# Optimization experiments

Hardware: AMD Instinct MI355X
Metric: run time of the kernel (lower is better)

Reference implementation:

```python
import jax, jax.numpy as jnp
import numpy as np

NV, NC = 4096, 16384        # n_vars, n_clauses
VL, CL = 8, 8               # vlabel_dim (ground_dim), clabel_dim
VE, CE = 128, 128           # vemb_dim, cemb_dim
ITERS = 4                   # max_iters
LN_EPS = 1e-5


def setup_inputs() -> dict:
    key = jax.random.key(0)
    ks = jax.random.split(key, 10)
    return {
        "vlabels": jax.random.normal(ks[0], (NV, VL), jnp.float32),
        "clabels": jax.random.normal(ks[1], (NC, CL), jnp.float32),
        "cmat_pos": jax.random.uniform(ks[2], (NC, NV), jnp.float32),
        "cmat_neg": jax.random.uniform(ks[3], (NC, NV), jnp.float32),
        "W_V_pos": jax.random.normal(ks[4], (VL + VE, CE), jnp.float32),
        "W_V_neg": jax.random.normal(ks[5], (VL + VE, CE), jnp.float32),
        "B_V": jax.random.normal(ks[6], (CE,), jnp.float32),
        "W_C_pos": jax.random.normal(ks[7], (CL + CE, VE), jnp.float32),
        "W_C_neg": jax.random.normal(ks[8], (CL + CE, VE), jnp.float32),
        "B_C": jax.random.normal(ks[9], (VE,), jnp.float32),
        "ln_gamma": jnp.ones((VE,), jnp.float32),
        "ln_beta": jnp.zeros((VE,), jnp.float32),
    }


def _layernorm(x, gamma, beta):
    mu = jnp.mean(x, axis=-1, keepdims=True)
    var = jnp.var(x, axis=-1, keepdims=True)
    return (x - mu) * jax.lax.rsqrt(var + LN_EPS) * gamma + beta


def reference(vlabels, clabels, cmat_pos, cmat_neg,
              W_V_pos, W_V_neg, B_V, W_C_pos, W_C_neg, B_C,
              ln_gamma, ln_beta):
    n_vars = vlabels.shape[0]
    vmat_pos = cmat_pos.T  # [NV, NC]
    vmat_neg = cmat_neg.T
    vembs0 = jnp.zeros((n_vars, VE), vlabels.dtype)

    def step(vembs, _):
        vs = jnp.concatenate([vlabels, vembs], axis=1)          # [NV, VL+VE]
        pv = vs @ W_V_pos                                       # [NV, CE]
        nv = vs @ W_V_neg
        cembs = jax.nn.relu(cmat_pos @ pv + cmat_neg @ nv + B_V)  # [NC, CE]
        cs = jnp.concatenate([clabels, cembs], axis=1)          # [NC, CL+CE]
        pc = cs @ W_C_pos                                       # [NC, VE]
        nc = cs @ W_C_neg
        v = jax.nn.relu(vmat_pos @ pc + vmat_neg @ nc + B_C)    # [NV, VE]
        v = _layernorm(v, ln_gamma, ln_beta)
        return v, None

    vembs, _ = jax.lax.scan(step, vembs0, None, length=ITERS)
    return vembs
```

## Files before the change

### kernel.cpp

```cpp
#include <hip/hip_runtime.h>

#define NVV 4096
#define NCC 16384
#define AS1 __attribute__((address_space(1)))
#define AS3 __attribute__((address_space(3)))

typedef __attribute__((ext_vector_type(8))) short short8;
typedef __attribute__((ext_vector_type(4))) short short4v;
typedef __attribute__((ext_vector_type(4))) float f32x4;

__device__ __forceinline__ short f2bf(float f) {
  union { float f; unsigned u; } v; v.f = f;
  unsigned r = v.u + 0x7fffu + ((v.u >> 16) & 1u);
  return (short)(r >> 16);
}

template<typename AT>
__device__ __forceinline__ short8 load8v(const AT* p) {
  if constexpr (sizeof(AT) == 2) {
    return *(const short8*)p;
  } else {
    const f32x4* q = (const f32x4*)p;
    f32x4 a = q[0], b = q[1];
    short8 o;
#pragma unroll
    for (int j = 0; j < 4; ++j) { o[j] = f2bf(a[j]); o[j + 4] = f2bf(b[j]); }
    return o;
  }
}

__global__ __launch_bounds__(256) void k_conv(const float* __restrict__ src,
                                              short* __restrict__ dst, int n8) {
  int i = blockIdx.x * blockDim.x + threadIdx.x;
  const int stride = gridDim.x * blockDim.x;
  for (; i < n8; i += stride) {
    const f32x4* q = (const f32x4*)(src + (size_t)i * 8);
    f32x4 a = q[0], b = q[1];
    short8 o;
#pragma unroll
    for (int j = 0; j < 4; ++j) { o[j] = f2bf(a[j]); o[j + 4] = f2bf(b[j]); }
    *(short8*)(dst + (size_t)i * 8) = o;
  }
}

__global__ __launch_bounds__(256) void k_convT(const float* __restrict__ src,
                                               short* __restrict__ dstN,
                                               short* __restrict__ dstT,
                                               int R, int C) {
  __shared__ short t[64][66];
  const int r0 = blockIdx.y * 64, c0 = blockIdx.x * 64;
  const int tr = threadIdx.x >> 2;
  const int q  = (threadIdx.x & 3) << 4;
  const float* s = src + (size_t)(r0 + tr) * C + c0 + q;
  const f32x4 v0 = *(const f32x4*)(s);
  const f32x4 v1 = *(const f32x4*)(s + 4);
  const f32x4 v2 = *(const f32x4*)(s + 8);
  const f32x4 v3 = *(const f32x4*)(s + 12);
  short8 a, b;
#pragma unroll
  for (int j = 0; j < 4; ++j) {
    a[j] = f2bf(v0[j]); a[4 + j] = f2bf(v1[j]);
    b[j] = f2bf(v2[j]); b[4 + j] = f2bf(v3[j]);
  }
  short* dn = dstN + (size_t)(r0 + tr) * C + c0 + q;
  *(short8*)dn = a;
  *(short8*)(dn + 8) = b;
#pragma unroll
  for (int j = 0; j < 8; ++j) { t[tr][q + j] = a[j]; t[tr][q + 8 + j] = b[j]; }
  __syncthreads();
  short8 oa, ob;
#pragma unroll
  for (int j = 0; j < 8; ++j) { oa[j] = t[q + j][tr]; ob[j] = t[q + 8 + j][tr]; }
  short* dt = dstT + (size_t)(c0 + tr) * R + r0 + q;
  *(short8*)dt = oa;
  *(short8*)(dt + 8) = ob;
}

template<int SRC, int NROW>
__global__ __launch_bounds__(128) void k_mlp(
    const float* __restrict__ labels, const float* __restrict__ embs,
    const float* __restrict__ bias,
    const float* __restrict__ Wp, const float* __restrict__ Wn,
    short* __restrict__ Tp, short* __restrict__ Tn, int Nrows, int KS) {
  __shared__ float xs[NROW][130];
  const int n = threadIdx.x;
  const int m0 = blockIdx.x * NROW;
  if (SRC == 2) {
#pragma unroll
    for (int r = 0; r < NROW; ++r) {
      const size_t m = m0 + r;
      float v = bias[n];
      for (int ks = 0; ks < KS; ++ks)
        v += embs[((size_t)ks * NCC + m) * 128 + n];
      xs[r][n] = fmaxf(v, 0.f);
    }
    __syncthreads();
  }
  float ap[NROW] = {}, an[NROW] = {};
  const int JMAX = (SRC == 0) ? 8 : 136;
  for (int j = 0; j < JMAX; ++j) {
    const float wp = Wp[j * 128 + n], wn = Wn[j * 128 + n];
#pragma unroll
    for (int r = 0; r < NROW; ++r) {
      float x;
      if (j < 8)            x = labels[(size_t)(m0 + r) * 8 + j];
      else if (SRC == 2)    x = xs[r][j - 8];
      else                  x = embs[(size_t)(m0 + r) * 128 + (j - 8)];
      ap[r] = fmaf(x, wp, ap[r]);
      an[r] = fmaf(x, wn, an[r]);
    }
  }
  short8 vp0, vn0, vp1, vn1;
#pragma unroll
  for (int r = 0; r < 8; ++r) {
    vp0[r] = f2bf(ap[r]); vn0[r] = f2bf(an[r]);
    vp1[r] = f2bf(ap[8 + r]); vn1[r] = f2bf(an[8 + r]);
  }
  *(short8*)(Tp + (size_t)n * Nrows + m0) = vp0;
  *(short8*)(Tp + (size_t)n * Nrows + m0 + 8) = vp1;
  *(short8*)(Tn + (size_t)n * Nrows + m0) = vn0;
  *(short8*)(Tn + (size_t)n * Nrows + m0 + 8) = vn1;
}

template<int EPI, int LSK>
__global__ __launch_bounds__(256, 1) void k_gemm6(
    const short* __restrict__ Ap, const short* __restrict__ An,
    const short* __restrict__ Bp, const short* __restrict__ Bn,
    const float* __restrict__ bias, float* __restrict__ C,
    int M, int lda, int ldb, int Klen) {
  __shared__ __align__(16) short sb[4][12288];
  const int tid = threadIdx.x;
  const int w = tid >> 6, l = tid & 63, lr = l & 15, lh = l >> 4;
  const int wr = w >> 1, wc = w & 1;
  const int id = blockIdx.x;
  const int zw = id & ((1 << LSK) - 1);
  const int xw = id >> LSK;
  const int m0 = xw * 64;
  const int Koff = zw * Klen;
  const int T = (Klen >> 6) << 1;

  const int srow = tid >> 3;
  const int scol = ((tid & 7) ^ (srow & 7)) << 3;
  const short* gAp = Ap + (size_t)(m0 + srow) * lda + Koff + scol;
  const short* gAn = An + (size_t)(m0 + srow) * lda + Koff + scol;
  const short* gBp = Bp + (size_t)srow * ldb + Koff + scol;
  const short* gBn = Bn + (size_t)srow * ldb + Koff + scol;

  f32x4 acc[2][4] = {};

  auto stage = [&](int t, int buf) {
    const int tt = (t < T) ? t : t - T;
    const int k0 = (tt >> 1) << 6;
    const short* A = (tt & 1) ? gAn : gAp;
    const short* B = (tt & 1) ? gBn : gBp;
#pragma unroll
    for (int i = 0; i < 2; ++i)
      __builtin_amdgcn_global_load_lds(
          (const AS1 void*)(A + (size_t)(i * 32) * lda + k0),
          (AS3 void*)(&sb[buf][i * 2048 + w * 512]), 16, 0, 0);
#pragma unroll
    for (int i = 0; i < 4; ++i)
      __builtin_amdgcn_global_load_lds(
          (const AS1 void*)(B + (size_t)(i * 32) * ldb + k0),
          (AS3 void*)(&sb[buf][4096 + i * 2048 + w * 512]), 16, 0, 0);
  };

  stage(0, 0);
  stage(1, 1);

  for (int t = 0; t < T; ++t) {
    stage(t + 2, (t + 2) & 3);
    asm volatile("s_waitcnt vmcnt(12)" ::: "memory");
    __builtin_amdgcn_s_barrier();
    asm volatile("" ::: "memory");
    const short* bp = &sb[t & 3][0];
#pragma unroll
    for (int kk = 0; kk < 2; ++kk) {
      const int kc = (kk << 2) + lh;
      short8 a[2], b[4];
#pragma unroll
      for (int mi = 0; mi < 2; ++mi) {
        const int row = (wr << 5) + (mi << 4) + lr;
        a[mi] = *(const short8*)&bp[(row << 6) + ((kc ^ (row & 7)) << 3)];
      }
#pragma unroll
      for (int nj = 0; nj < 4; ++nj) {
        const int n = (wc << 6) + (nj << 4) + lr;
        b[nj] = *(const short8*)&bp[4096 + (n << 6) + ((kc ^ (n & 7)) << 3)];
      }
#pragma unroll
      for (int mi = 0; mi < 2; ++mi)
#pragma unroll
        for (int nj = 0; nj < 4; ++nj)
          acc[mi][nj] = __builtin_amdgcn_mfma_f32_16x16x32_bf16(
              a[mi], b[nj], acc[mi][nj], 0, 0, 0);
    }
  }

#pragma unroll
  for (int mi = 0; mi < 2; ++mi)
#pragma unroll
    for (int nj = 0; nj < 4; ++nj) {
      const int col = (wc << 6) + (nj << 4) + lr;
#pragma unroll
      for (int r = 0; r < 4; ++r) {
        const int m = m0 + (wr << 5) + (mi << 4) + (lh << 2) + r;
        if (EPI == 0) {
          C[(size_t)m * 128 + col] = fmaxf(acc[mi][nj][r] + bias[col], 0.f);
        } else {
          C[((size_t)zw * M + m) * 128 + col] = acc[mi][nj][r];
        }
      }
    }
}

template<typename AT, bool TRANSA, int EPI>
__global__ __launch_bounds__(256) void k_gemm(
    const AT* __restrict__ Ap, const AT* __restrict__ An,
    const short* __restrict__ Bp, const short* __restrict__ Bn,
    const float* __restrict__ bias, float* __restrict__ C,
    int M, int lda, int ldb, int Klen) {
  __shared__ __align__(16) short sA[2][32 * 64];
  __shared__ __align__(16) short sB[2][64 * 64];
  const int tid = threadIdx.x;
  const int w = tid >> 6, l = tid & 63, lr = l & 15, lh = l >> 4;
  const int m0 = blockIdx.x * 32, n0 = blockIdx.y * 64;
  const int Koff = blockIdx.z * Klen;
  f32x4 acc0 = {0.f, 0.f, 0.f, 0.f}, acc1 = {0.f, 0.f, 0.f, 0.f};

  for (int step = 0; step < (Klen >> 6); ++step) {
    const int k0 = Koff + (step << 6);
    __syncthreads();
    if (!TRANSA) {
      const int m = tid >> 3, kc = tid & 7;
      const size_t ga = (size_t)(m0 + m) * lda + k0 + (kc << 3);
      const int ad = (m << 6) + ((kc ^ (m & 7)) << 3);
      *(short8*)&sA[0][ad] = load8v(Ap + ga);
      *(short8*)&sA[1][ad] = load8v(An + ga);
    } else {
      const int r = tid >> 2, c8 = (tid & 3) << 3;
      const size_t ga = (size_t)(k0 + r) * lda + m0 + c8;
      short8 vp = load8v(Ap + ga), vn = load8v(An + ga);
#pragma unroll
      for (int j = 0; j < 8; ++j) {
        const int m = c8 + j;
        const int ad = (m << 6) + ((((r >> 3)) ^ (m & 7)) << 3) + (r & 7);
        sA[0][ad] = vp[j];
        sA[1][ad] = vn[j];
      }
    }
#pragma unroll
    for (int i = 0; i < 2; ++i) {
      const int c = (i << 8) + tid;
      const int n = c >> 3, kc = c & 7;
      const size_t gb = (size_t)(n0 + n) * ldb + k0 + (kc << 3);
      const int ad = (n << 6) + ((kc ^ (n & 7)) << 3);
      *(short8*)&sB[0][ad] = *(const short8*)(Bp + gb);
      *(short8*)&sB[1][ad] = *(const short8*)(Bn + gb);
    }
    __syncthreads();
#pragma unroll
    for (int kh = 0; kh < 2; ++kh) {
      const int kc = (kh << 2) + lh;
      const int bn_ = (w << 4) + lr;
      short8 bpv = *(short8*)&sB[0][(bn_ << 6) + ((kc ^ (bn_ & 7)) << 3)];
      short8 bnv = *(short8*)&sB[1][(bn_ << 6) + ((kc ^ (bn_ & 7)) << 3)];
      short8 a0p = *(short8*)&sA[0][(lr << 6) + ((kc ^ (lr & 7)) << 3)];
      short8 a0n = *(short8*)&sA[1][(lr << 6) + ((kc ^ (lr & 7)) << 3)];
      const int m1 = 16 + lr;
      short8 a1p = *(short8*)&sA[0][(m1 << 6) + ((kc ^ (m1 & 7)) << 3)];
      short8 a1n = *(short8*)&sA[1][(m1 << 6) + ((kc ^ (m1 & 7)) << 3)];
      acc0 = __builtin_amdgcn_mfma_f32_16x16x32_bf16(a0p, bpv, acc0, 0, 0, 0);
      acc0 = __builtin_amdgcn_mfma_f32_16x16x32_bf16(a0n, bnv, acc0, 0, 0, 0);
      acc1 = __builtin_amdgcn_mfma_f32_16x16x32_bf16(a1p, bpv, acc1, 0, 0, 0);
      acc1 = __builtin_amdgcn_mfma_f32_16x16x32_bf16(a1n, bnv, acc1, 0, 0, 0);
    }
  }
  const int n = n0 + (w << 4) + lr;
#pragma unroll
  for (int mf = 0; mf < 2; ++mf) {
    f32x4 a = mf ? acc1 : acc0;
#pragma unroll
    for (int r = 0; r < 4; ++r) {
      const int m = m0 + (mf << 4) + (lh << 2) + r;
      float c = a[r];
      if (EPI == 0) {
        c += bias[n];
        c = fmaxf(c, 0.f);
        C[(size_t)m * 128 + n] = c;
      } else {
        C[((size_t)blockIdx.z * M + m) * 128 + n] = c;
      }
    }
  }
}

template<int KS>
__global__ __launch_bounds__(256) void k_reduce_ln(
    const float* __restrict__ part, const float* __restrict__ bias,
    const float* __restrict__ gamma, const float* __restrict__ beta,
    float* __restrict__ out) {
  const int w = threadIdx.x >> 6, l = threadIdx.x & 63;
  const int m = blockIdx.x * 4 + w;
  const int n0 = l << 1;
  float x0 = bias[n0], x1 = bias[n0 + 1];
#pragma unroll
  for (int ks = 0; ks < KS; ++ks) {
    const size_t o = ((size_t)ks * NVV + m) * 128 + n0;
    x0 += part[o];
    x1 += part[o + 1];
  }
  x0 = fmaxf(x0, 0.f);
  x1 = fmaxf(x1, 0.f);
  float s = x0 + x1, q = x0 * x0 + x1 * x1;
#pragma unroll
  for (int off = 32; off; off >>= 1) {
    s += __shfl_xor(s, off);
    q += __shfl_xor(q, off);
  }
  const float mu = s * (1.f / 128.f);
  const float var = q * (1.f / 128.f) - mu * mu;
  const float inv = 1.f / sqrtf(var + 1e-5f);
  out[(size_t)m * 128 + n0]     = (x0 - mu) * inv * gamma[n0] + beta[n0];
  out[(size_t)m * 128 + n0 + 1] = (x1 - mu) * inv * gamma[n0 + 1] + beta[n0 + 1];
}

extern "C" void kernel_launch(void* const* d_in, const int* in_sizes, int n_in,
                              void* d_out, int out_size, void* d_ws, size_t ws_size,
                              hipStream_t stream) {
  const float* vlabels  = (const float*)d_in[0];
  const float* clabels  = (const float*)d_in[1];
  const float* cmat_pos = (const float*)d_in[2];
  const float* cmat_neg = (const float*)d_in[3];
  const float* Wvp = (const float*)d_in[4];
  const float* Wvn = (const float*)d_in[5];
  const float* Bv  = (const float*)d_in[6];
  const float* Wcp = (const float*)d_in[7];
  const float* Wcn = (const float*)d_in[8];
  const float* Bc  = (const float*)d_in[9];
  const float* gam = (const float*)d_in[10];
  const float* bet = (const float*)d_in[11];
  float* out = (float*)d_out;

  char* base = (char*)d_ws;
  const size_t SZ_vT = (size_t)128 * NVV * 2;
  const size_t SZ_cT = (size_t)128 * NCC * 2;
  const size_t SZ_cm = (size_t)NCC * NVV * 2;
  const size_t SZ_p8 = (size_t)NCC * 128 * 4;

  size_t o = 0;
  auto al = [&](size_t b) { size_t p = o; o += (b + 255) & ~(size_t)255; return p; };

  short* pvT  = (short*)(base + al(SZ_vT));
  short* nvT  = (short*)(base + al(SZ_vT));
  short* pcT  = (short*)(base + al(SZ_cT));
  short* ncT  = (short*)(base + al(SZ_cT));
  float* scr8 = (float*)(base + al(SZ_p8));
  short* cmPb = (short*)(base + al(SZ_cm));
  short* cmNb = (short*)(base + al(SZ_cm));
  short* cmTP = (short*)(base + al(SZ_cm));
  short* cmTN = (short*)(base + al(SZ_cm));
  const size_t needF = o;

  if (ws_size >= needF) {
    k_convT<<<dim3(NVV / 64, NCC / 64), 256, 0, stream>>>(cmat_pos, cmPb, cmTP, NCC, NVV);
    k_convT<<<dim3(NVV / 64, NCC / 64), 256, 0, stream>>>(cmat_neg, cmNb, cmTN, NCC, NVV);

    for (int it = 0; it < 4; ++it) {
      if (it == 0)
        k_mlp<0, 16><<<NVV / 16, 128, 0, stream>>>(vlabels, nullptr, nullptr, Wvp, Wvn, pvT, nvT, NVV, 0);
      else
        k_mlp<1, 16><<<NVV / 16, 128, 0, stream>>>(vlabels, out, nullptr, Wvp, Wvn, pvT, nvT, NVV, 0);

      k_gemm6<0, 0><<<NCC / 64, 256, 0, stream>>>(
          cmPb, cmNb, pvT, nvT, Bv, scr8, NCC, NVV, NVV, NVV);

      k_mlp<1, 16><<<NCC / 16, 128, 0, stream>>>(clabels, scr8, nullptr, Wcp, Wcn, pcT, ncT, NCC, 0);

      k_gemm6<1, 2><<<(NVV / 64) * 4, 256, 0, stream>>>(
          cmTP, cmTN, pcT, ncT, nullptr, scr8, NVV, NCC, NCC, NCC / 4);

      k_reduce_ln<4><<<NVV / 4, 256, 0, stream>>>(scr8, Bc, gam, bet, out);
    }
    return;
  }

  o = 0;
  pvT = (short*)(base + al(SZ_vT));
  nvT = (short*)(base + al(SZ_vT));
  pcT = (short*)(base + al(SZ_cT));
  ncT = (short*)(base + al(SZ_cT));
  float* part = (float*)(base + al(2 * SZ_p8));
  float* cemb = (float*)(base + al(SZ_p8));
  cmPb = (short*)(base + al(SZ_cm));
  cmNb = (short*)(base + al(SZ_cm));
  const size_t needN = o;
  const bool big = ws_size >= needN;

  if (big) {
    k_conv<<<4096, 256, 0, stream>>>(cmat_pos, cmPb, NCC * NVV / 8);
    k_conv<<<4096, 256, 0, stream>>>(cmat_neg, cmNb, NCC * NVV / 8);
  }

  for (int it = 0; it < 4; ++it) {
    if (it == 0)
      k_mlp<0, 16><<<NVV / 16, 128, 0, stream>>>(vlabels, nullptr, nullptr, Wvp, Wvn, pvT, nvT, NVV, 0);
    else
      k_mlp<1, 16><<<NVV / 16, 128, 0, stream>>>(vlabels, out, nullptr, Wvp, Wvn, pvT, nvT, NVV, 0);

    if (big) {
      k_gemm<short, false, 0><<<dim3(NCC / 32, 2, 1), 256, 0, stream>>>(
          cmPb, cmNb, pvT, nvT, Bv, cemb, NCC, NVV, NVV, NVV);
      k_mlp<1, 16><<<NCC / 16, 128, 0, stream>>>(clabels, cemb, nullptr, Wcp, Wcn, pcT, ncT, NCC, 0);
      k_gemm<short, true, 1><<<dim3(NVV / 32, 2, 4), 256, 0, stream>>>(
          cmPb, cmNb, pcT, ncT, nullptr, part, NVV, NVV, NCC, NVV);
      k_reduce_ln<4><<<NVV / 4, 256, 0, stream>>>(part, Bc, gam, bet, out);
    } else {
      k_gemm<float, false, 0><<<dim3(NCC / 32, 2, 1), 256, 0, stream>>>(
          cmat_pos, cmat_neg, pvT, nvT, Bv, cemb, NCC, NVV, NVV, NVV);
      k_mlp<1, 16><<<NCC / 16, 128, 0, stream>>>(clabels, cemb, nullptr, Wcp, Wcn, pcT, ncT, NCC, 0);
      k_gemm<float, true, 1><<<dim3(NVV / 32, 2, 4), 256, 0, stream>>>(
          cmat_pos, cmat_neg, pcT, ncT, nullptr, part, NVV, NVV, NCC, NVV);
      k_reduce_ln<4><<<NVV / 4, 256, 0, stream>>>(part, Bc, gam, bet, out);
    }
  }
}
```

Baseline: 1.382 ms.

## Replace GEMM with 128-row tiles, split-K for both passes, fused pos/neg stages

The bf16 MFMA GEMM now uses 128x128 output tiles with K-step 32, double-buffered LDS, and loads both pos and neg A/B tiles into each stage. Occupancy is raised to 2 blocks per CU. Both sparse-style products now use split-K (4 and 16 ways), which puts 512 blocks on the GPU. The clause bias+ReLU moves into the MLP kernel, which reduces the partials. The MLP kernel also stages embeddings through LDS. The costs are larger partial-sum scratch buffers and extra reduction traffic, and each step waits on vmcnt(0), so loads overlap with compute less.

```diff
diff --git a/kernel.cpp b/kernel.cpp
--- a/kernel.cpp
+++ b/kernel.cpp
@@ -82,10 +82,15 @@
     const float* __restrict__ bias,
     const float* __restrict__ Wp, const float* __restrict__ Wn,
     short* __restrict__ Tp, short* __restrict__ Tn, int Nrows, int KS) {
-  __shared__ float xs[NROW][130];
+  __shared__ float xs[NROW][129];
   const int n = threadIdx.x;
   const int m0 = blockIdx.x * NROW;
-  if (SRC == 2) {
+  if (SRC == 1) {
+#pragma unroll
+    for (int r = 0; r < NROW; ++r)
+      xs[r][n] = embs[(size_t)(m0 + r) * 128 + n];
+    __syncthreads();
+  } else if (SRC == 2) {
 #pragma unroll
     for (int r = 0; r < NROW; ++r) {
       const size_t m = m0 + r;
@@ -103,9 +108,8 @@
 #pragma unroll
     for (int r = 0; r < NROW; ++r) {
       float x;
-      if (j < 8)            x = labels[(size_t)(m0 + r) * 8 + j];
-      else if (SRC == 2)    x = xs[r][j - 8];
-      else                  x = embs[(size_t)(m0 + r) * 128 + (j - 8)];
+      if (j < 8) x = labels[(size_t)(m0 + r) * 8 + j];
+      else       x = xs[r][j - 8];
       ap[r] = fmaf(x, wp, ap[r]);
       an[r] = fmaf(x, wn, an[r]);
     }
@@ -122,94 +126,94 @@
   *(short8*)(Tn + (size_t)n * Nrows + m0 + 8) = vn1;
 }
 
-template<int EPI, int LSK>
-__global__ __launch_bounds__(256, 1) void k_gemm6(
+template<int LSK>
+__global__ __launch_bounds__(256, 2) void k_gemm8(
     const short* __restrict__ Ap, const short* __restrict__ An,
     const short* __restrict__ Bp, const short* __restrict__ Bn,
-    const float* __restrict__ bias, float* __restrict__ C,
-    int M, int lda, int ldb, int Klen) {
-  __shared__ __align__(16) short sb[4][12288];
+    float* __restrict__ C, int M, int lda, int ldb, int Klen) {
+  __shared__ __align__(16) short sb[2][16384];
   const int tid = threadIdx.x;
   const int w = tid >> 6, l = tid & 63, lr = l & 15, lh = l >> 4;
   const int wr = w >> 1, wc = w & 1;
   const int id = blockIdx.x;
   const int zw = id & ((1 << LSK) - 1);
-  const int xw = id >> LSK;
-  const int m0 = xw * 64;
+  const int m0 = (id >> LSK) * 128;
   const int Koff = zw * Klen;
-  const int T = (Klen >> 6) << 1;
-
-  const int srow = tid >> 3;
-  const int scol = ((tid & 7) ^ (srow & 7)) << 3;
+  const int T = Klen >> 5;
+
+  const int srow = (w << 4) + (l >> 2);
+  const int scol = ((l & 3) ^ (srow & 3)) << 3;
   const short* gAp = Ap + (size_t)(m0 + srow) * lda + Koff + scol;
   const short* gAn = An + (size_t)(m0 + srow) * lda + Koff + scol;
   const short* gBp = Bp + (size_t)srow * ldb + Koff + scol;
   const short* gBn = Bn + (size_t)srow * ldb + Koff + scol;
 
-  f32x4 acc[2][4] = {};
-
-  auto stage = [&](int t, int buf) {
-    const int tt = (t < T) ? t : t - T;
-    const int k0 = (tt >> 1) << 6;
-    const short* A = (tt & 1) ? gAn : gAp;
-    const short* B = (tt & 1) ? gBn : gBp;
-#pragma unroll
-    for (int i = 0; i < 2; ++i)
-      __builtin_amdgcn_global_load_lds(
-          (const AS1 void*)(A + (size_t)(i * 32) * lda + k0),
-          (AS3 void*)(&sb[buf][i * 2048 + w * 512]), 16, 0, 0);
-#pragma unroll
-    for (int i = 0; i < 4; ++i)
-      __builtin_amdgcn_global_load_lds(
-          (const AS1 void*)(B + (size_t)(i * 32) * ldb + k0),
-          (AS3 void*)(&sb[buf][4096 + i * 2048 + w * 512]), 16, 0, 0);
+  f32x4 acc[4][4] = {};
+
+  auto stage = [&](int kstep, int buf) {
+    const int k0 = kstep << 5;
+    short* db = &sb[buf][0];
+#pragma unroll
+    for (int i = 0; i < 2; ++i) {
+      const size_t ra = (size_t)(i * 64) * lda + k0;
+      const size_t rb = (size_t)(i * 64) * ldb + k0;
+      const int d = (i * 256 + w * 64) * 8;
+      __builtin_amdgcn_global_load_lds((const AS1 void*)(gAp + ra),
+                                       (AS3 void*)(db + d), 16, 0, 0);
+      __builtin_amdgcn_global_load_lds((const AS1 void*)(gAn + ra),
+                                       (AS3 void*)(db + 4096 + d), 16, 0, 0);
+      __builtin_amdgcn_global_load_lds((const AS1 void*)(gBp + rb),
+                                       (AS3 void*)(db + 8192 + d), 16, 0, 0);
+      __builtin_amdgcn_global_load_lds((const AS1 void*)(gBn + rb),
+                                       (AS3 void*)(db + 12288 + d), 16, 0, 0);
+    }
   };
 
   stage(0, 0);
-  stage(1, 1);
+  asm volatile("s_waitcnt vmcnt(0)" ::: "memory");
+  __builtin_amdgcn_s_barrier();
+  asm volatile("" ::: "memory");
 
   for (int t = 0; t < T; ++t) {
-    stage(t + 2, (t + 2) & 3);
-    asm volatile("s_waitcnt vmcnt(12)" ::: "memory");
+    stage((t + 1 < T) ? t + 1 : 0, (t + 1) & 1);
+    const short* bp = &sb[t & 1][0];
+    short8 a[2][4], b[2][4];
+#pragma unroll
+    for (int mi = 0; mi < 4; ++mi) {
+      const int row = (wr << 6) + (mi << 4) + lr;
+      const int ad = (row << 5) + ((lh ^ (row & 3)) << 3);
+      a[0][mi] = *(const short8*)&bp[ad];
+      a[1][mi] = *(const short8*)&bp[4096 + ad];
+    }
+#pragma unroll
+    for (int nj = 0; nj < 4; ++nj) {
+      const int n = (wc << 6) + (nj << 4) + lr;
+      const int bd = (n << 5) + ((lh ^ (n & 3)) << 3);
+      b[0][nj] = *(const short8*)&bp[8192 + bd];
+      b[1][nj] = *(const short8*)&bp[12288 + bd];
+    }
+#pragma unroll
+    for (int mat = 0; mat < 2; ++mat)
+#pragma unroll
+      for (int mi = 0; mi < 4; ++mi)
+#pragma unroll
+        for (int nj = 0; nj < 4; ++nj)
+          acc[mi][nj] = __builtin_amdgcn_mfma_f32_16x16x32_bf16(
+              a[mat][mi], b[mat][nj], acc[mi][nj], 0, 0, 0);
+    asm volatile("s_waitcnt vmcnt(0)" ::: "memory");
     __builtin_amdgcn_s_barrier();
     asm volatile("" ::: "memory");
-    const short* bp = &sb[t & 3][0];
-#pragma unroll
-    for (int kk = 0; kk < 2; ++kk) {
-      const int kc = (kk << 2) + lh;
-      short8 a[2], b[4];
-#pragma unroll
-      for (int mi = 0; mi < 2; ++mi) {
-        const int row = (wr << 5) + (mi << 4) + lr;
-        a[mi] = *(const short8*)&bp[(row << 6) + ((kc ^ (row & 7)) << 3)];
-      }
-#pragma unroll
-      for (int nj = 0; nj < 4; ++nj) {
-        const int n = (wc << 6) + (nj << 4) + lr;
-        b[nj] = *(const short8*)&bp[4096 + (n << 6) + ((kc ^ (n & 7)) << 3)];
-      }
-#pragma unroll
-      for (int mi = 0; mi < 2; ++mi)
-#pragma unroll
-        for (int nj = 0; nj < 4; ++nj)
-          acc[mi][nj] = __builtin_amdgcn_mfma_f32_16x16x32_bf16(
-              a[mi], b[nj], acc[mi][nj], 0, 0, 0);
-    }
-  }
-
-#pragma unroll
-  for (int mi = 0; mi < 2; ++mi)
+  }
+
+#pragma unroll
+  for (int mi = 0; mi < 4; ++mi)
 #pragma unroll
     for (int nj = 0; nj < 4; ++nj) {
       const int col = (wc << 6) + (nj << 4) + lr;
 #pragma unroll
       for (int r = 0; r < 4; ++r) {
-        const int m = m0 + (wr << 5) + (mi << 4) + (lh << 2) + r;
-        if (EPI == 0) {
-          C[(size_t)m * 128 + col] = fmaxf(acc[mi][nj][r] + bias[col], 0.f);
-        } else {
-          C[((size_t)zw * M + m) * 128 + col] = acc[mi][nj][r];
-        }
+        const int m = m0 + (wr << 6) + (mi << 4) + (lh << 2) + r;
+        C[((size_t)zw * M + m) * 128 + col] = acc[mi][nj][r];
       }
     }
 }
@@ -355,7 +359,7 @@
   short* nvT  = (short*)(base + al(SZ_vT));
   short* pcT  = (short*)(base + al(SZ_cT));
   short* ncT  = (short*)(base + al(SZ_cT));
-  float* scr8 = (float*)(base + al(SZ_p8));
+  float* scr  = (float*)(base + al(4 * SZ_p8));
   short* cmPb = (short*)(base + al(SZ_cm));
   short* cmNb = (short*)(base + al(SZ_cm));
   short* cmTP = (short*)(base + al(SZ_cm));
@@ -372,15 +376,13 @@
       else
         k_mlp<1, 16><<<NVV / 16, 128, 0, stream>>>(vlabels, out, nullptr, Wvp, Wvn, pvT, nvT, NVV, 0);
 
-      k_gemm6<0, 0><<<NCC / 64, 256, 0, stream>>>(
-          cmPb, cmNb, pvT, nvT, Bv, scr8, NCC, NVV, NVV, NVV);
-
-      k_mlp<1, 16><<<NCC / 16, 128, 0, stream>>>(clabels, scr8, nullptr, Wcp, Wcn, pcT, ncT, NCC, 0);
-
-      k_gemm6<1, 2><<<(NVV / 64) * 4, 256, 0, stream>>>(
-          cmTP, cmTN, pcT, ncT, nullptr, scr8, NVV, NCC, NCC, NCC / 4);
-
-      k_reduce_ln<4><<<NVV / 4, 256, 0, stream>>>(scr8, Bc, gam, bet, out);
+      k_gemm8<2><<<512, 256, 0, stream>>>(
+          cmPb, cmNb, pvT, nvT, scr, NCC, NVV, NVV, NVV / 4);
+      k_mlp<2, 16><<<NCC / 16, 128, 0, stream>>>(clabels, scr, Bv, Wcp, Wcn, pcT, ncT, NCC, 4);
+
+      k_gemm8<4><<<512, 256, 0, stream>>>(
+          cmTP, cmTN, pcT, ncT, scr, NVV, NCC, NCC, NCC / 16);
+      k_reduce_ln<16><<<NVV / 4, 256, 0, stream>>>(scr, Bc, gam, bet, out);
     }
     return;
   }
```

Measured after the change: 1.558 ms. +12.8%, slower.

## Split-K both GEMMs to 512 blocks with 3-stage pipeline and 2 blocks/CU

Applied to the files above, without the earlier changes.

The clause GEMM becomes split-K by 2, with bias and relu applied in the following MLP, which sums the partials. The variable GEMM becomes split-K by 8 instead of 4. Each launch now uses 512 blocks, so work spreads across more CUs. The LDS ring drops from 4 to 3 buffers with prefetch depth 1 so that two blocks fit per CU, and the MLP stages vembs into shared memory. The cost is extra partial-sum traffic and reduction work, plus a shallower prefetch that may expose load latency.

```diff
diff --git a/kernel.cpp b/kernel.cpp
--- a/kernel.cpp
+++ b/kernel.cpp
@@ -82,10 +82,15 @@
     const float* __restrict__ bias,
     const float* __restrict__ Wp, const float* __restrict__ Wn,
     short* __restrict__ Tp, short* __restrict__ Tn, int Nrows, int KS) {
-  __shared__ float xs[NROW][130];
+  __shared__ float xs[NROW][129];
   const int n = threadIdx.x;
   const int m0 = blockIdx.x * NROW;
-  if (SRC == 2) {
+  if (SRC == 1) {
+#pragma unroll
+    for (int r = 0; r < NROW; ++r)
+      xs[r][n] = embs[(size_t)(m0 + r) * 128 + n];
+    __syncthreads();
+  } else if (SRC == 2) {
 #pragma unroll
     for (int r = 0; r < NROW; ++r) {
       const size_t m = m0 + r;
@@ -103,9 +108,8 @@
 #pragma unroll
     for (int r = 0; r < NROW; ++r) {
       float x;
-      if (j < 8)            x = labels[(size_t)(m0 + r) * 8 + j];
-      else if (SRC == 2)    x = xs[r][j - 8];
-      else                  x = embs[(size_t)(m0 + r) * 128 + (j - 8)];
+      if (j < 8) x = labels[(size_t)(m0 + r) * 8 + j];
+      else       x = xs[r][j - 8];
       ap[r] = fmaf(x, wp, ap[r]);
       an[r] = fmaf(x, wn, an[r]);
     }
@@ -123,19 +127,18 @@
 }
 
 template<int EPI, int LSK>
-__global__ __launch_bounds__(256, 1) void k_gemm6(
+__global__ __launch_bounds__(256, 2) void k_gemm10(
     const short* __restrict__ Ap, const short* __restrict__ An,
     const short* __restrict__ Bp, const short* __restrict__ Bn,
     const float* __restrict__ bias, float* __restrict__ C,
     int M, int lda, int ldb, int Klen) {
-  __shared__ __align__(16) short sb[4][12288];
+  __shared__ __align__(16) short sb[3][12288];
   const int tid = threadIdx.x;
   const int w = tid >> 6, l = tid & 63, lr = l & 15, lh = l >> 4;
   const int wr = w >> 1, wc = w & 1;
   const int id = blockIdx.x;
   const int zw = id & ((1 << LSK) - 1);
-  const int xw = id >> LSK;
-  const int m0 = xw * 64;
+  const int m0 = (id >> LSK) * 64;
   const int Koff = zw * Klen;
   const int T = (Klen >> 6) << 1;
 
@@ -166,14 +169,16 @@
   };
 
   stage(0, 0);
-  stage(1, 1);
-
+
+  int bufc = 0;
+  const int r0 = lr, r1 = 16 + lr;
   for (int t = 0; t < T; ++t) {
-    stage(t + 2, (t + 2) & 3);
-    asm volatile("s_waitcnt vmcnt(12)" ::: "memory");
+    const int bufn = (bufc == 2) ? 0 : bufc + 1;
+    stage(t + 1, bufn);
+    asm volatile("s_waitcnt vmcnt(6)" ::: "memory");
     __builtin_amdgcn_s_barrier();
     asm volatile("" ::: "memory");
-    const short* bp = &sb[t & 3][0];
+    const short* bp = &sb[bufc][0];
 #pragma unroll
     for (int kk = 0; kk < 2; ++kk) {
       const int kc = (kk << 2) + lh;
@@ -195,7 +200,9 @@
           acc[mi][nj] = __builtin_amdgcn_mfma_f32_16x16x32_bf16(
               a[mi], b[nj], acc[mi][nj], 0, 0, 0);
     }
-  }
+    bufc = bufn;
+  }
+  (void)r0; (void)r1;
 
 #pragma unroll
   for (int mi = 0; mi < 2; ++mi)
@@ -355,7 +362,7 @@
   short* nvT  = (short*)(base + al(SZ_vT));
   short* pcT  = (short*)(base + al(SZ_cT));
   short* ncT  = (short*)(base + al(SZ_cT));
-  float* scr8 = (float*)(base + al(SZ_p8));
+  float* scr  = (float*)(base + al(2 * SZ_p8));
   short* cmPb = (short*)(base + al(SZ_cm));
   short* cmNb = (short*)(base + al(SZ_cm));
   short* cmTP = (short*)(base + al(SZ_cm));
@@ -372,15 +379,13 @@
       else
         k_mlp<1, 16><<<NVV / 16, 128, 0, stream>>>(vlabels, out, nullptr, Wvp, Wvn, pvT, nvT, NVV, 0);
 
-      k_gemm6<0, 0><<<NCC / 64, 256, 0, stream>>>(
-          cmPb, cmNb, pvT, nvT, Bv, scr8, NCC, NVV, NVV, NVV);
-
-      k_mlp<1, 16><<<NCC / 16, 128, 0, stream>>>(clabels, scr8, nullptr, Wcp, Wcn, pcT, ncT, NCC, 0);
-
-      k_gemm6<1, 2><<<(NVV / 64) * 4, 256, 0, stream>>>(
-          cmTP, cmTN, pcT, ncT, nullptr, scr8, NVV, NCC, NCC, NCC / 4);
-
-      k_reduce_ln<4><<<NVV / 4, 256, 0, stream>>>(scr8, Bc, gam, bet, out);
+      k_gemm10<1, 1><<<512, 256, 0, stream>>>(
+          cmPb, cmNb, pvT, nvT, nullptr, scr, NCC, NVV, NVV, NVV / 2);
+      k_mlp<2, 16><<<NCC / 16, 128, 0, stream>>>(clabels, scr, Bv, Wcp, Wcn, pcT, ncT, NCC, 2);
+
+      k_gemm10<1, 3><<<512, 256, 0, stream>>>(
+          cmTP, cmTN, pcT, ncT, nullptr, scr, NVV, NCC, NCC, NCC / 8);
+      k_reduce_ln<8><<<NVV / 4, 256, 0, stream>>>(scr, Bc, gam, bet, out);
     }
     return;
   }
```

Result: slower. 1.493 ms (+8.1%).
